# Optimization experiments

Measured on AMD Instinct MI355X. Metric: run time of the kernel, lower is better.

Reference implementation:

```python
import jax, jax.numpy as jnp
import numpy as np

B, S, H = 8, 2048, 512
DK = 512


def setup_inputs() -> dict:
    key = jax.random.key(0)
    ks = jax.random.split(key, 10)
    inp = {
        "X": jax.random.normal(ks[0], (B, S, H), dtype=jnp.float32),
        "event_flag": jax.random.uniform(ks[1], (B, S, 1), dtype=jnp.float32),
        "lengths": jax.random.randint(ks[2], (B,), 1, S + 1),
        # Linear params (torch Linear: y = x @ W.T + b, W is [out,in])
        "Wq": jax.random.normal(ks[3], (H, H), dtype=jnp.float32) / np.sqrt(H),
        "bq": jnp.zeros((H,), dtype=jnp.float32),
        "Wk": jax.random.normal(ks[4], (H, H), dtype=jnp.float32) / np.sqrt(H),
        "bk": jnp.zeros((H,), dtype=jnp.float32),
        "Wv": jax.random.normal(ks[5], (H, H), dtype=jnp.float32) / np.sqrt(H),
        "bv": jnp.zeros((H,), dtype=jnp.float32),
        "event_weight": jnp.zeros((1,), dtype=jnp.float32),
        "shape_ratio": jnp.ones((1,), dtype=jnp.float32),
    }
    return inp


def reference(X, event_flag, lengths, Wq, bq, Wk, bk, Wv, bv, event_weight, shape_ratio):
    # QKV projections: [B,S,H]
    Q = jnp.einsum("bsh,oh->bso", X, Wq) + bq
    K = jnp.einsum("bsh,oh->bso", X, Wk) + bk
    V = jnp.einsum("bsh,oh->bso", X, Wv) + bv
    # scaled scores [B,S,S], learned shape_ratio scale
    scores = jnp.einsum("bqh,bkh->bqk", Q, K) / jnp.sqrt(jnp.float32(DK))
    scores = scores * shape_ratio
    # event_flag [B,S,1] broadcasts over last (key) dim: per-query additive bias
    scores = scores + event_weight * event_flag
    attn = jax.nn.softmax(scores, axis=-1)
    context = jnp.einsum("bqk,bkh->bqh", attn, V)
    return context, attn
```

## Files before the change

kernel.cpp:

```cpp
#include <hip/hip_runtime.h>
#include <stdint.h>


#define Bn 8
#define Sn 2048
#define Hn 512
#define BM 128
#define BN 128
#define BKk 64

typedef unsigned short u16;
typedef _Float16 h16;
typedef __attribute__((ext_vector_type(8))) _Float16 f16x8;
typedef __attribute__((ext_vector_type(4))) _Float16 f16x4;
typedef __attribute__((ext_vector_type(4))) float f32x4;

__device__ __forceinline__ f32x4 mfma16h(f16x8 a, f16x8 b, f32x4 c) {
  return __builtin_amdgcn_mfma_f32_16x16x32_f16(a, b, c, 0, 0, 0);
}
__device__ __forceinline__ void g2l16(const void* g, void* l) {
  __builtin_amdgcn_global_load_lds(
      (const __attribute__((address_space(1))) void*)g,
      (__attribute__((address_space(3))) void*)l,
      16, 0, 0);
}

__global__ __launch_bounds__(256) void k0_cvt(
    const float* __restrict__ X,
    const float* __restrict__ Wq, const float* __restrict__ Wk,
    const float* __restrict__ Wv,
    h16* __restrict__ Xf, h16* __restrict__ Wf) {
  const int y = blockIdx.y;
  const float* src;
  h16* dst;
  int n;
  if (y == 0) {
    src = X; dst = Xf; n = 16384 * 512;
  } else {
    src = (y == 1) ? Wq : ((y == 2) ? Wk : Wv);
    dst = Wf + (size_t)(y - 1) * 512 * 512;
    n = 512 * 512;
  }
  const int i = (blockIdx.x * 256 + threadIdx.x) * 8;
  if (i >= n) return;
  float4 v0 = *(const float4*)(src + i);
  float4 v1 = *(const float4*)(src + i + 4);
  f16x8 h;
  h[0] = (h16)v0.x; h[1] = (h16)v0.y; h[2] = (h16)v0.z; h[3] = (h16)v0.w;
  h[4] = (h16)v1.x; h[5] = (h16)v1.y; h[6] = (h16)v1.z; h[7] = (h16)v1.w;
  *(f16x8*)(dst + i) = h;
}

__global__ __launch_bounds__(256) void k1_proj(
    const h16* __restrict__ Xf, const h16* __restrict__ Wf,
    const float* __restrict__ bq, const float* __restrict__ bk,
    const float* __restrict__ bv,
    h16* __restrict__ Qf, h16* __restrict__ Kf, h16* __restrict__ Vt) {
  __shared__ h16 lA[BM * BKk], lB[BM * BKk];
  const int t = threadIdx.x;
  const int lane = t & 63;
  const int wid = t >> 6;
  const int wr = wid >> 1, wc = wid & 1;
  const int l = blockIdx.x;
  const int xcd = l & 7;
  const int slot = l >> 3;
  const int m_idx = xcd * 16 + slot / 12;
  const int tn = slot % 12;
  const int m0 = m_idx * BM;
  const int mat = tn >> 2;
  const int o0 = (tn & 3) * BN;
  const float* bsel = (mat == 0) ? bq : ((mat == 1) ? bk : bv);
  const size_t arow0 = (size_t)m0;
  const size_t brow0 = (size_t)mat * 512 + o0;

  f32x4 acc[4][4];
  const f32x4 fz = {0.f, 0.f, 0.f, 0.f};
#pragma unroll
  for (int m = 0; m < 4; ++m)
#pragma unroll
    for (int n = 0; n < 4; ++n) acc[m][n] = fz;

  const int srow = lane >> 3;
  const int scol = ((lane & 7) ^ srow) << 3;

  for (int k0 = 0; k0 < Hn; k0 += BKk) {
    __syncthreads();
#pragma unroll
    for (int j = 0; j < 4; ++j) {
      const int ci = wid * 4 + j;
      const int row = ci * 8 + srow;
      g2l16(Xf + (arow0 + row) * Hn + k0 + scol, &lA[ci * 512]);
      g2l16(Wf + (brow0 + row) * Hn + k0 + scol, &lB[ci * 512]);
    }
    __syncthreads();
#pragma unroll
    for (int ks = 0; ks < 2; ++ks) {
      f16x8 af[4], bf[4];
#pragma unroll
      for (int m = 0; m < 4; ++m) {
        const int row = wr * 64 + m * 16 + (lane & 15);
        const int col8 = ks * 4 + (lane >> 4);
        af[m] = *(const f16x8*)&lA[row * BKk + ((col8 ^ (row & 7)) << 3)];
      }
#pragma unroll
      for (int n = 0; n < 4; ++n) {
        const int row = wc * 64 + n * 16 + (lane & 15);
        const int col8 = ks * 4 + (lane >> 4);
        bf[n] = *(const f16x8*)&lB[row * BKk + ((col8 ^ (row & 7)) << 3)];
      }
#pragma unroll
      for (int m = 0; m < 4; ++m)
#pragma unroll
        for (int n = 0; n < 4; ++n)
          acc[m][n] = mfma16h(af[m], bf[n], acc[m][n]);
    }
  }
#pragma unroll
  for (int n = 0; n < 4; ++n) {
    const int o = o0 + wc * 64 + n * 16 + (lane & 15);
    const float bias = bsel[o];
#pragma unroll
    for (int m = 0; m < 4; ++m) {
      const int ib = m0 + wr * 64 + m * 16 + ((lane >> 4) << 2);
      if (mat < 2) {
        h16* Dst = (mat == 0) ? Qf : Kf;
#pragma unroll
        for (int r = 0; r < 4; ++r)
          Dst[(size_t)(ib + r) * Hn + o] = (h16)(acc[m][n][r] + bias);
      } else {
        const int bb = ib >> 11, s = ib & 2047;
        f16x4 p;
#pragma unroll
        for (int r = 0; r < 4; ++r) p[r] = (h16)(acc[m][n][r] + bias);
        *(f16x4*)&Vt[((size_t)bb * Hn + o) * Sn + s] = p;
      }
    }
  }
}

__global__ __launch_bounds__(256) void k2_scores(
    const h16* __restrict__ Qf, const h16* __restrict__ Kf,
    const float* __restrict__ shape_ratio,
    h16* __restrict__ S16, float* __restrict__ Par) {
  __shared__ h16 lA[BM * BKk], lB[BM * BKk];
  const int t = threadIdx.x;
  const int lane = t & 63;
  const int wid = t >> 6;
  const int wr = wid >> 1, wc = wid & 1;
  const int l = blockIdx.x;
  const int b = l & 7;
  const int slot = l >> 3;
  const int mi = slot >> 4;
  const int ni = slot & 15;
  const int n0 = ni * BN;
  const int m0 = mi * BM;
  const size_t qrow0 = (size_t)b * Sn + m0;
  const size_t krow0 = (size_t)b * Sn + n0;

  f32x4 acc[4][4];
  const f32x4 fz = {0.f, 0.f, 0.f, 0.f};
#pragma unroll
  for (int m = 0; m < 4; ++m)
#pragma unroll
    for (int n = 0; n < 4; ++n) acc[m][n] = fz;

  const int srow = lane >> 3;
  const int scol = ((lane & 7) ^ srow) << 3;

  for (int k0 = 0; k0 < Hn; k0 += BKk) {
    __syncthreads();
#pragma unroll
    for (int j = 0; j < 4; ++j) {
      const int ci = wid * 4 + j;
      const int row = ci * 8 + srow;
      g2l16(Qf + (qrow0 + row) * Hn + k0 + scol, &lA[ci * 512]);
      g2l16(Kf + (krow0 + row) * Hn + k0 + scol, &lB[ci * 512]);
    }
    __syncthreads();
#pragma unroll
    for (int ks = 0; ks < 2; ++ks) {
      f16x8 af[4], bf[4];
#pragma unroll
      for (int m = 0; m < 4; ++m) {
        const int row = wr * 64 + m * 16 + (lane & 15);
        const int col8 = ks * 4 + (lane >> 4);
        af[m] = *(const f16x8*)&lA[row * BKk + ((col8 ^ (row & 7)) << 3)];
      }
#pragma unroll
      for (int n = 0; n < 4; ++n) {
        const int row = wc * 64 + n * 16 + (lane & 15);
        const int col8 = ks * 4 + (lane >> 4);
        bf[n] = *(const f16x8*)&lB[row * BKk + ((col8 ^ (row & 7)) << 3)];
      }
#pragma unroll
      for (int m = 0; m < 4; ++m)
#pragma unroll
        for (int n = 0; n < 4; ++n)
          acc[m][n] = mfma16h(af[m], bf[n], acc[m][n]);
    }
  }
  const float scale = shape_ratio[0] * 0.044194173824159216f;
  float psum[4][4];
#pragma unroll
  for (int m = 0; m < 4; ++m)
#pragma unroll
    for (int r = 0; r < 4; ++r) psum[m][r] = 0.f;

#pragma unroll
  for (int n = 0; n < 4; ++n) {
    const int kk = n0 + wc * 64 + n * 16 + (lane & 15);
#pragma unroll
    for (int m = 0; m < 4; ++m) {
      const int q = m0 + wr * 64 + m * 16 + ((lane >> 4) << 2);
#pragma unroll
      for (int r = 0; r < 4; ++r) {
        const float e = __expf(acc[m][n][r] * scale);
        S16[((size_t)b * Sn + q + r) * 4096 + 2048 + kk] = (h16)e;
        psum[m][r] += e;
      }
    }
  }
#pragma unroll
  for (int m = 0; m < 4; ++m)
#pragma unroll
    for (int r = 0; r < 4; ++r) {
      float s = psum[m][r];
      s += __shfl_xor(s, 1);
      s += __shfl_xor(s, 2);
      s += __shfl_xor(s, 4);
      s += __shfl_xor(s, 8);
      psum[m][r] = s;
    }
  if ((lane & 15) == 0) {
    const int pslot = ni * 2 + wc;
#pragma unroll
    for (int m = 0; m < 4; ++m) {
      const int q = m0 + wr * 64 + m * 16 + ((lane >> 4) << 2);
#pragma unroll
      for (int r = 0; r < 4; ++r)
        Par[((size_t)b * Sn + q + r) * 32 + pslot] = psum[m][r];
    }
  }
}

__global__ __launch_bounds__(256) void k4_pv(
    const h16* __restrict__ S16, const float* __restrict__ Par,
    const h16* __restrict__ Vt, float* __restrict__ Ctx) {
  __shared__ h16 lA[BM * BKk], lB[BM * BKk];
  __shared__ float invSh[BM];
  const int t = threadIdx.x;
  const int lane = t & 63;
  const int wid = t >> 6;
  const int wr = wid >> 1, wc = wid & 1;
  const int l = blockIdx.x;
  const int b = l & 7;
  const int slot = l >> 3;
  const int mi = slot >> 2;
  const int ni = slot & 3;
  const int n0 = ni * BN;
  const int m0 = mi * BM;

  if (t < BM) {
    const float* p = Par + ((size_t)b * Sn + m0 + t) * 32;
    float s = 0.f;
#pragma unroll
    for (int i = 0; i < 32; ++i) s += p[i];
    invSh[t] = 1.0f / s;
  }

  f32x4 acc[4][4];
  const f32x4 fz = {0.f, 0.f, 0.f, 0.f};
#pragma unroll
  for (int m = 0; m < 4; ++m)
#pragma unroll
    for (int n = 0; n < 4; ++n) acc[m][n] = fz;

  const int srow = lane >> 3;
  const int scol = ((lane & 7) ^ srow) << 3;

  for (int k0 = 0; k0 < Sn; k0 += BKk) {
    __syncthreads();
#pragma unroll
    for (int j = 0; j < 4; ++j) {
      const int ci = wid * 4 + j;
      const int row = ci * 8 + srow;
      g2l16(S16 + ((size_t)(b * Sn + m0 + row)) * 4096 + 2048 + k0 + scol,
            &lA[ci * 512]);
      g2l16(Vt + ((size_t)b * Hn + n0 + row) * Sn + k0 + scol, &lB[ci * 512]);
    }
    __syncthreads();
#pragma unroll
    for (int ks = 0; ks < 2; ++ks) {
      f16x8 af[4], bf[4];
#pragma unroll
      for (int m = 0; m < 4; ++m) {
        const int row = wr * 64 + m * 16 + (lane & 15);
        const int col8 = ks * 4 + (lane >> 4);
        af[m] = *(const f16x8*)&lA[row * BKk + ((col8 ^ (row & 7)) << 3)];
      }
#pragma unroll
      for (int n = 0; n < 4; ++n) {
        const int row = wc * 64 + n * 16 + (lane & 15);
        const int col8 = ks * 4 + (lane >> 4);
        bf[n] = *(const f16x8*)&lB[row * BKk + ((col8 ^ (row & 7)) << 3)];
      }
#pragma unroll
      for (int m = 0; m < 4; ++m)
#pragma unroll
        for (int n = 0; n < 4; ++n)
          acc[m][n] = mfma16h(af[m], bf[n], acc[m][n]);
    }
  }
#pragma unroll
  for (int n = 0; n < 4; ++n) {
    const int h = n0 + wc * 64 + n * 16 + (lane & 15);
#pragma unroll
    for (int m = 0; m < 4; ++m) {
      const int qb = wr * 64 + m * 16 + ((lane >> 4) << 2);
#pragma unroll
      for (int r = 0; r < 4; ++r)
        Ctx[((size_t)(b * Sn + m0 + qb + r)) * Hn + h] =
            acc[m][n][r] * invSh[qb + r];
    }
  }
}

__global__ __launch_bounds__(256) void k3_norm(
    const float* __restrict__ Par, float* __restrict__ attnF) {
  const int r = blockIdx.x;
  const int t = threadIdx.x;
  float* row = attnF + (size_t)r * Sn;
  const h16* erow = (const h16*)row + 2048;

  f16x8 e = *(const f16x8*)(erow + t * 8);

  __shared__ float shInv;
  float s = (t < 32) ? Par[(size_t)r * 32 + t] : 0.f;
  if (t < 64) {
    s += __shfl_xor(s, 32);
    s += __shfl_xor(s, 16);
    s += __shfl_xor(s, 8);
    s += __shfl_xor(s, 4);
    s += __shfl_xor(s, 2);
    s += __shfl_xor(s, 1);
    if (t == 0) shInv = 1.0f / s;
  }
  __syncthreads();
  const float iv = shInv;

  float4 o0 = make_float4((float)e[0] * iv, (float)e[1] * iv,
                          (float)e[2] * iv, (float)e[3] * iv);
  float4 o1 = make_float4((float)e[4] * iv, (float)e[5] * iv,
                          (float)e[6] * iv, (float)e[7] * iv);
  *(float4*)(row + t * 8) = o0;
  *(float4*)(row + t * 8 + 4) = o1;
}

extern "C" void kernel_launch(void* const* d_in, const int* in_sizes, int n_in,
                              void* d_out, int out_size, void* d_ws, size_t ws_size,
                              hipStream_t stream) {
  const float* X  = (const float*)d_in[0];
  const float* Wq = (const float*)d_in[3];
  const float* bq = (const float*)d_in[4];
  const float* Wk = (const float*)d_in[5];
  const float* bk = (const float*)d_in[6];
  const float* Wv = (const float*)d_in[7];
  const float* bv = (const float*)d_in[8];
  const float* shape_ratio = (const float*)d_in[10];

  float* ctx  = (float*)d_out;
  float* attn = ctx + (size_t)Bn * Sn * Hn;

  h16* ws = (h16*)d_ws;
  const size_t A = (size_t)Bn * Sn * Hn;
  const size_t W3 = (size_t)3 * 512 * 512;
  h16* Xf = ws;
  h16* Wf = ws + A;
  h16* Qf = ws + A + W3;
  h16* Kf = ws + 2 * A + W3;
  float* Par = (float*)(ws + 3 * A + W3);
  h16* Vt = ws + 4 * A;

  k0_cvt<<<dim3(4096, 4), 256, 0, stream>>>(X, Wq, Wk, Wv, Xf, Wf);
  k1_proj<<<dim3(1536), 256, 0, stream>>>(Xf, Wf, bq, bk, bv, Qf, Kf, Vt);
  k2_scores<<<dim3(2048), 256, 0, stream>>>(Qf, Kf, shape_ratio,
                                            (h16*)attn, Par);
  k4_pv<<<dim3(512), 256, 0, stream>>>((const h16*)attn, Par, Vt, ctx);
  k3_norm<<<dim3(Bn * Sn), 256, 0, stream>>>(Par, attn);
}
```

Baseline: 190.5 us.

## Fuse attention normalization into PV kernel using separate workspace exp buffer

```diff
diff --git a/kernel.cpp b/kernel.cpp
--- a/kernel.cpp
+++ b/kernel.cpp
@@ -141,7 +141,8 @@
 __global__ __launch_bounds__(256) void k2_scores(
     const h16* __restrict__ Qf, const h16* __restrict__ Kf,
     const float* __restrict__ shape_ratio,
-    h16* __restrict__ S16, float* __restrict__ Par) {
+    h16* __restrict__ Ep, size_t estride, int eoff,
+    float* __restrict__ Par) {
   __shared__ h16 lA[BM * BKk], lB[BM * BKk];
   const int t = threadIdx.x;
   const int lane = t & 63;
@@ -215,7 +216,7 @@
 #pragma unroll
       for (int r = 0; r < 4; ++r) {
         const float e = __expf(acc[m][n][r] * scale);
-        S16[((size_t)b * Sn + q + r) * 4096 + 2048 + kk] = (h16)e;
+        Ep[((size_t)b * Sn + q + r) * estride + eoff + kk] = (h16)e;
         psum[m][r] += e;
       }
     }
@@ -244,8 +245,9 @@
 }
 
 __global__ __launch_bounds__(256) void k4_pv(
-    const h16* __restrict__ S16, const float* __restrict__ Par,
-    const h16* __restrict__ Vt, float* __restrict__ Ctx) {
+    const h16* __restrict__ Ep, size_t estride, int eoff,
+    const float* __restrict__ Par, const h16* __restrict__ Vt,
+    float* __restrict__ Ctx, float* __restrict__ attnF, int writeAttn) {
   __shared__ h16 lA[BM * BKk], lB[BM * BKk];
   __shared__ float invSh[BM];
   const int t = threadIdx.x;
@@ -284,7 +286,7 @@
     for (int j = 0; j < 4; ++j) {
       const int ci = wid * 4 + j;
       const int row = ci * 8 + srow;
-      g2l16(S16 + ((size_t)(b * Sn + m0 + row)) * 4096 + 2048 + k0 + scol,
+      g2l16(Ep + ((size_t)(b * Sn + m0 + row)) * estride + eoff + k0 + scol,
             &lA[ci * 512]);
       g2l16(Vt + ((size_t)b * Hn + n0 + row) * Sn + k0 + scol, &lB[ci * 512]);
     }
@@ -309,6 +311,25 @@
 #pragma unroll
         for (int n = 0; n < 4; ++n)
           acc[m][n] = mfma16h(af[m], bf[n], acc[m][n]);
+    }
+    if (writeAttn && (k0 >> 9) == ni) {
+      const int row = t >> 1;
+      const int cb = (t & 1) * 4;
+      const float iv = invSh[row];
+      float* dst =
+          attnF + ((size_t)(b * Sn + m0 + row)) * Sn + k0 + (t & 1) * 32;
+#pragma unroll
+      for (int cc = 0; cc < 4; ++cc) {
+        const int col8 = cb + cc;
+        const f16x8 e =
+            *(const f16x8*)&lA[row * BKk + ((col8 ^ (row & 7)) << 3)];
+        float4 o0 = make_float4((float)e[0] * iv, (float)e[1] * iv,
+                                (float)e[2] * iv, (float)e[3] * iv);
+        float4 o1 = make_float4((float)e[4] * iv, (float)e[5] * iv,
+                                (float)e[6] * iv, (float)e[7] * iv);
+        *(float4*)(dst + cc * 8) = o0;
+        *(float4*)(dst + cc * 8 + 4) = o1;
+      }
     }
   }
 #pragma unroll
@@ -381,10 +402,23 @@
   float* Par = (float*)(ws + 3 * A + W3);
   h16* Vt = ws + 4 * A;
 
+  const bool bigWs = ws_size >= (size_t)9 * A * 2;
+
   k0_cvt<<<dim3(4096, 4), 256, 0, stream>>>(X, Wq, Wk, Wv, Xf, Wf);
   k1_proj<<<dim3(1536), 256, 0, stream>>>(Xf, Wf, bq, bk, bv, Qf, Kf, Vt);
-  k2_scores<<<dim3(2048), 256, 0, stream>>>(Qf, Kf, shape_ratio,
-                                            (h16*)attn, Par);
-  k4_pv<<<dim3(512), 256, 0, stream>>>((const h16*)attn, Par, Vt, ctx);
-  k3_norm<<<dim3(Bn * Sn), 256, 0, stream>>>(Par, attn);
-}
+
+  if (bigWs) {
+    h16* Ep = ws + 5 * A;
+    k2_scores<<<dim3(2048), 256, 0, stream>>>(Qf, Kf, shape_ratio,
+                                              Ep, (size_t)Sn, 0, Par);
+    k4_pv<<<dim3(512), 256, 0, stream>>>(Ep, (size_t)Sn, 0, Par, Vt,
+                                         ctx, attn, 1);
+  } else {
+    k2_scores<<<dim3(2048), 256, 0, stream>>>(Qf, Kf, shape_ratio,
+                                              (h16*)attn, (size_t)4096, 2048,
+                                              Par);
+    k4_pv<<<dim3(512), 256, 0, stream>>>((const h16*)attn, (size_t)4096, 2048,
+                                         Par, Vt, ctx, attn, 0);
+    k3_norm<<<dim3(Bn * Sn), 256, 0, stream>>>(Par, attn);
+  }
+}
```

Result: slower. 197.1 us (+3.5%).
